# Kernel optimization log

Measured on AMD Instinct MI355X. Metric: run time of the kernel, lower is better.

Reference implementation:

```python
import jax, jax.numpy as jnp
import numpy as np

EPS = 1e-6
TEMPERATURE = 0.1
NEG_INF = -1.0e9

B, S, H = 8, 1024, 1024
M = 16384  # memory_size


def setup_inputs() -> dict:
    key = jax.random.key(0)
    ks = jax.random.split(key, 10)
    sc = 1.0 / np.sqrt(H)
    return {
        "hidden_states": jax.random.normal(ks[0], (B, S, H), jnp.float32),
        "Wk": jax.random.normal(ks[1], (H, H), jnp.float32) * sc,
        "bk": jax.random.normal(ks[2], (H,), jnp.float32) * 0.01,
        "Wv": jax.random.normal(ks[3], (H, H), jnp.float32) * sc,
        "bv": jax.random.normal(ks[4], (H,), jnp.float32) * 0.01,
        "Wo": jax.random.normal(ks[5], (H, H), jnp.float32) * sc,
        "bo": jax.random.normal(ks[6], (H,), jnp.float32) * 0.01,
        "memory_keys": jax.random.normal(ks[7], (M, H), jnp.float32),
        "memory_values": jax.random.normal(ks[8], (M, H), jnp.float32),
        "memory_usage": jax.random.randint(ks[9], (M,), 0, 3, jnp.int32),
    }


def _normalize(x):
    # matches torch: x * rsqrt(sum(x^2) + 1e-6)
    return x * jax.lax.rsqrt(jnp.sum(jnp.square(x), axis=-1, keepdims=True) + EPS)


def reference(hidden_states, Wk, bk, Wv, bv, Wo, bo,
              memory_keys, memory_values, memory_usage):
    # key projection + L2-ish normalization of queries
    q = hidden_states @ Wk.T + bk              # [B,S,H]
    qn = _normalize(q)
    mkn = _normalize(memory_keys)              # [M,H]
    # cosine-similarity attention over memory slots
    scores = jnp.einsum('bsh,mh->bsm', qn, mkn) / TEMPERATURE  # [B,S,M]
    mask = (memory_usage > 0).astype(scores.dtype)             # [M]
    scores = scores * mask + NEG_INF * (1.0 - mask)
    w = jax.nn.softmax(scores, axis=-1)                        # [B,S,M]
    retrieved = jnp.einsum('bsm,mh->bsh', w, memory_values)    # [B,S,H]
    return retrieved @ Wo.T + bo
```

## Files before the change

### kernel.cpp

```cpp
#include <hip/hip_runtime.h>
#include <hip/hip_bf16.h>
#include <stdint.h>
#include <stddef.h>

typedef __bf16 bf16_t;
typedef __attribute__((ext_vector_type(8))) __bf16 bf16x8;
typedef __attribute__((ext_vector_type(4))) __bf16 bf16x4;
typedef __attribute__((ext_vector_type(4))) float f32x4;

#define HDIM 1024
#define MSLOTS 16384
#define NROWS 8192

__device__ __forceinline__ void load16_lds(const void* g, void* l) {
  __builtin_amdgcn_global_load_lds((const __attribute__((address_space(1))) void*)g,
                                   (__attribute__((address_space(3))) void*)l, 16, 0, 0);
}

__global__ void init_compact(int* __restrict__ cmask) {
  int i = blockIdx.x * blockDim.x + threadIdx.x;
  if (i < MSLOTS) cmask[i] = 0;
}

__global__ void compact_scan(const int* __restrict__ usage, int* __restrict__ posmap,
                             int* __restrict__ cmask, int* __restrict__ smalls) {
  __shared__ int wtot[16], wbase[16];
  const int t = threadIdx.x;
  const int lane = t & 63, wid = t >> 6;
  const int base = t * 16;
  unsigned mask = 0;
  int c = 0;
  #pragma unroll
  for (int i = 0; i < 16; ++i) {
    if (usage[base + i] > 0) { mask |= (1u << i); ++c; }
  }
  int inc = c;
  #pragma unroll
  for (int d = 1; d < 64; d <<= 1) {
    int n = __shfl_up(inc, d);
    if (lane >= d) inc += n;
  }
  if (lane == 63) wtot[wid] = inc;
  __syncthreads();
  if (t == 0) {
    int acc = 0;
    #pragma unroll
    for (int w = 0; w < 16; ++w) { wbase[w] = acc; acc += wtot[w]; }
    smalls[0] = acc;
    smalls[1] = ((acc + 511) >> 9) << 9;
  }
  __syncthreads();
  int pos = wbase[wid] + inc - c;
  #pragma unroll
  for (int i = 0; i < 16; ++i) {
    if ((mask >> i) & 1u) {
      posmap[pos] = base + i;
      cmask[pos] = 1;
      ++pos;
    }
  }
}

__global__ void cvt_f32_bf16(const float* __restrict__ X, bf16_t* __restrict__ Y, int n8) {
  int i = blockIdx.x * blockDim.x + threadIdx.x;
  if (i >= n8) return;
  float4 a = ((const float4*)X)[2 * i];
  float4 b = ((const float4*)X)[2 * i + 1];
  bf16x8 o;
  o[0] = (bf16_t)a.x; o[1] = (bf16_t)a.y; o[2] = (bf16_t)a.z; o[3] = (bf16_t)a.w;
  o[4] = (bf16_t)b.x; o[5] = (bf16_t)b.y; o[6] = (bf16_t)b.z; o[7] = (bf16_t)b.w;
  ((bf16x8*)Y)[i] = o;
}

__global__ void normalize_rows(const float* __restrict__ X, bf16_t* __restrict__ Y) {
  __shared__ float part[4];
  const int t = threadIdx.x;
  const size_t row = blockIdx.x;
  float4 v = ((const float4*)(X + row * 1024))[t];
  float s = v.x * v.x + v.y * v.y + v.z * v.z + v.w * v.w;
  #pragma unroll
  for (int m = 32; m >= 1; m >>= 1) s += __shfl_xor(s, m);
  if ((t & 63) == 0) part[t >> 6] = s;
  __syncthreads();
  float tot = part[0] + part[1] + part[2] + part[3];
  float r = rsqrtf(tot + 1e-6f);
  bf16x4 o;
  o[0] = (bf16_t)(v.x * r); o[1] = (bf16_t)(v.y * r);
  o[2] = (bf16_t)(v.z * r); o[3] = (bf16_t)(v.w * r);
  *(bf16x4*)&Y[row * 1024 + t * 4] = o;
}

__global__ void normalize_gather(const float* __restrict__ mk, const int* __restrict__ posmap,
                                 const int* __restrict__ smalls, bf16_t* __restrict__ cmkn) {
  __shared__ float part[4];
  const int p = blockIdx.x;
  const int cnt = smalls[0], mpad = smalls[1];
  if (p >= mpad) return;
  const int t = threadIdx.x;
  if (p >= cnt) {
    bf16x4 z;
    z[0] = z[1] = z[2] = z[3] = (bf16_t)0.f;
    *(bf16x4*)&cmkn[(size_t)p * 1024 + t * 4] = z;
    return;
  }
  const int slot = posmap[p];
  float4 v = ((const float4*)(mk + (size_t)slot * 1024))[t];
  float s = v.x * v.x + v.y * v.y + v.z * v.z + v.w * v.w;
  #pragma unroll
  for (int m = 32; m >= 1; m >>= 1) s += __shfl_xor(s, m);
  if ((t & 63) == 0) part[t >> 6] = s;
  __syncthreads();
  float tot = part[0] + part[1] + part[2] + part[3];
  float r = rsqrtf(tot + 1e-6f);
  bf16x4 o;
  o[0] = (bf16_t)(v.x * r); o[1] = (bf16_t)(v.y * r);
  o[2] = (bf16_t)(v.z * r); o[3] = (bf16_t)(v.w * r);
  *(bf16x4*)&cmkn[(size_t)p * 1024 + t * 4] = o;
}

__global__ void transpose_gather(const float* __restrict__ mv, const int* __restrict__ posmap,
                                 const int* __restrict__ smalls, bf16_t* __restrict__ cVt) {
  __shared__ float tile[32][33];
  const int cnt = smalls[0], mpad = smalls[1];
  const int p0 = blockIdx.y * 32;
  if (p0 >= mpad) return;
  const int tx = threadIdx.x & 31, ty = threadIdx.x >> 5;
  const int h0 = blockIdx.x * 32;
  #pragma unroll
  for (int j = 0; j < 32; j += 8) {
    const int pos = p0 + ty + j;
    float val = 0.f;
    if (pos < cnt) val = mv[(size_t)posmap[pos] * 1024 + h0 + tx];
    tile[ty + j][tx] = val;
  }
  __syncthreads();
  #pragma unroll
  for (int j = 0; j < 32; j += 8)
    cVt[(size_t)(h0 + ty + j) * MSLOTS + p0 + tx] = (bf16_t)tile[tx][ty + j];
}

__global__ void zero_f32(float* __restrict__ p, int n4) {
  int i = blockIdx.x * blockDim.x + threadIdx.x;
  if (i < n4) ((float4*)p)[i] = (float4){0.f, 0.f, 0.f, 0.f};
}

__global__ void scale_cvt(const float* __restrict__ retrf, const float* __restrict__ den,
                          bf16_t* __restrict__ out, int n4) {
  int i = blockIdx.x * blockDim.x + threadIdx.x;
  if (i >= n4) return;
  float4 s = ((const float4*)retrf)[i];
  const int row = (i * 4) >> 10;
  const float r = 1.0f / den[row];
  bf16x4 o;
  o[0] = (bf16_t)(s.x * r); o[1] = (bf16_t)(s.y * r);
  o[2] = (bf16_t)(s.z * r); o[3] = (bf16_t)(s.w * r);
  ((bf16x4*)out)[i] = o;
}

__global__ void reduce_scale(const float* __restrict__ part, size_t partStride, int ks,
                             const float* __restrict__ den, bf16_t* __restrict__ out, int n4) {
  int i = blockIdx.x * blockDim.x + threadIdx.x;
  if (i >= n4) return;
  float4 s = ((const float4*)part)[i];
  for (int k = 1; k < ks; ++k) {
    float4 t = ((const float4*)(part + (size_t)k * partStride))[i];
    s.x += t.x; s.y += t.y; s.z += t.z; s.w += t.w;
  }
  const int row = (i * 4) >> 10;
  const float r = 1.0f / den[row];
  bf16x4 o;
  o[0] = (bf16_t)(s.x * r); o[1] = (bf16_t)(s.y * r);
  o[2] = (bf16_t)(s.z * r); o[3] = (bf16_t)(s.w * r);
  ((bf16x4*)out)[i] = o;
}

template <int EPI>
__global__ void gemm_bt(const bf16_t* __restrict__ A, const bf16_t* __restrict__ Bt,
                        int ldk, int kLenIn, int ldc,
                        const float* __restrict__ bias,
                        const int* __restrict__ cmask,
                        float* __restrict__ den,
                        float* __restrict__ outf, bf16_t* __restrict__ outb,
                        const int* __restrict__ smalls, int ks, size_t partStride) {
  __shared__ bf16_t lA[128 * 32];
  __shared__ bf16_t lB[128 * 32];
  const int t = threadIdx.x;
  const int lane = t & 63;
  const int wave = t >> 6;
  const int wm = (wave >> 1) << 6;
  const int wn = (wave & 1) << 6;
  const int lr = lane & 15;
  const int lq = lane >> 4;

  int bx = blockIdx.x, by = blockIdx.y, bz = blockIdx.z;
  {
    const unsigned nx = gridDim.x, ny = gridDim.y;
    if ((ny & 7u) == 0u) {
      unsigned lin = blockIdx.x + nx * (blockIdx.y + ny * blockIdx.z);
      unsigned ylow = lin & 7u;
      lin >>= 3;
      const unsigned nyh = ny >> 3;
      unsigned yhigh = lin % nyh;
      lin /= nyh;
      bx = lin % nx;
      bz = lin / nx;
      by = ylow + 8u * yhigh;
    }
  }

  int kLen = kLenIn;
  int kstart = 0;
  if (EPI == 1) {
    if (bx * 128 >= smalls[1]) return;
  }
  if (EPI == 3 || EPI == 4) {
    kLen = smalls[1] / ks;
    kstart = bz * kLen;
  }

  const int r0 = t >> 2;
  const int c0 = (t & 3) * 8;
  const bf16_t* pA0 = A + (size_t)(by * 128 + r0) * ldk + kstart + c0;
  const bf16_t* pA1 = pA0 + (size_t)64 * ldk;
  const bf16_t* pB0 = Bt + (size_t)(bx * 128 + r0) * ldk + kstart + c0;
  const bf16_t* pB1 = pB0 + (size_t)64 * ldk;

  f32x4 acc[4][4];
  #pragma unroll
  for (int i = 0; i < 4; ++i)
    #pragma unroll
    for (int j = 0; j < 4; ++j) acc[i][j] = (f32x4){0.f, 0.f, 0.f, 0.f};

  for (int k0 = 0; k0 < kLen; k0 += 32) {
    __syncthreads();
    load16_lds(pA0, &lA[t * 8]);
    load16_lds(pA1, &lA[2048 + t * 8]);
    load16_lds(pB0, &lB[t * 8]);
    load16_lds(pB1, &lB[2048 + t * 8]);
    pA0 += 32; pA1 += 32; pB0 += 32; pB1 += 32;
    __syncthreads();
    bf16x8 af[4], bfr[4];
    #pragma unroll
    for (int i = 0; i < 4; ++i)
      af[i] = *(const bf16x8*)&lA[(wm + i * 16 + lr) * 32 + lq * 8];
    #pragma unroll
    for (int j = 0; j < 4; ++j)
      bfr[j] = *(const bf16x8*)&lB[(wn + j * 16 + lr) * 32 + lq * 8];
    #pragma unroll
    for (int i = 0; i < 4; ++i)
      #pragma unroll
      for (int j = 0; j < 4; ++j)
        acc[i][j] = __builtin_amdgcn_mfma_f32_16x16x32_bf16(af[i], bfr[j], acc[i][j], 0, 0, 0);
  }

  const int colBase = bx * 128 + wn + lr;
  const int rowBase = by * 128 + wm + lq * 4;

  if (EPI == 4) outf += (size_t)bz * partStride;

  float rs[4][4];
  if (EPI == 1) {
    #pragma unroll
    for (int i = 0; i < 4; ++i)
      #pragma unroll
      for (int r = 0; r < 4; ++r) rs[i][r] = 0.f;
  }

  #pragma unroll
  for (int j = 0; j < 4; ++j) {
    const int col = colBase + j * 16;
    float bval = 0.f;
    bool ok = true;
    if (EPI == 0) bval = bias[col];
    if (EPI == 1) ok = cmask[col] > 0;
    #pragma unroll
    for (int i = 0; i < 4; ++i) {
      const int row = rowBase + i * 16;
      #pragma unroll
      for (int r = 0; r < 4; ++r) {
        const size_t idx = (size_t)(row + r) * ldc + col;
        float v = acc[i][j][r];
        if (EPI == 0) outf[idx] = v + bval;
        if (EPI == 1) {
          float e = ok ? exp2f(v * 14.426950408889634f) : 0.f;
          rs[i][r] += e;
          outb[idx] = (bf16_t)e;
        }
        if (EPI == 3) atomicAdd(&outf[idx], v);
        if (EPI == 4) outf[idx] = v;
      }
    }
  }

  if (EPI == 1) {
    #pragma unroll
    for (int i = 0; i < 4; ++i)
      #pragma unroll
      for (int r = 0; r < 4; ++r) {
        float s = rs[i][r];
        s += __shfl_xor(s, 1);
        s += __shfl_xor(s, 2);
        s += __shfl_xor(s, 4);
        s += __shfl_xor(s, 8);
        if (lr == 0) atomicAdd(&den[rowBase + i * 16 + r], s);
      }
  }
}

extern "C" void kernel_launch(void* const* d_in, const int* in_sizes, int n_in,
                              void* d_out, int out_size, void* d_ws, size_t ws_size,
                              hipStream_t stream) {
  const float* hs = (const float*)d_in[0];
  const float* Wk = (const float*)d_in[1];
  const float* bk = (const float*)d_in[2];
  const float* Wo = (const float*)d_in[5];
  const float* bo = (const float*)d_in[6];
  const float* mk = (const float*)d_in[7];
  const float* mv = (const float*)d_in[8];
  const int* usage = (const int*)d_in[9];
  float* out = (float*)d_out;

  char* ws = (char*)d_ws;
  size_t off = 0;
  auto alloc = [&](size_t b) -> void* {
    void* p = ws + off;
    off += (b + 255) & ~(size_t)255;
    return p;
  };
  bf16_t* cmkn = (bf16_t*)alloc((size_t)MSLOTS * HDIM * 2);
  bf16_t* cVt = (bf16_t*)alloc((size_t)HDIM * MSLOTS * 2);
  bf16_t* qnb = (bf16_t*)alloc((size_t)NROWS * HDIM * 2);
  bf16_t* retrb = (bf16_t*)alloc((size_t)NROWS * HDIM * 2);
  bf16_t* Wob = (bf16_t*)alloc((size_t)HDIM * HDIM * 2);
  float* den = (float*)alloc((size_t)NROWS * 4);
  int* posmap = (int*)alloc((size_t)MSLOTS * 4);
  int* cmask = (int*)alloc((size_t)MSLOTS * 4);
  int* smalls = (int*)alloc(256 * 4);
  const size_t fixed = off;

  int chunk = 128, ksplit = 4, partialMode = 0;
  {
    const int cc[8] = {4096, 4096, 2048, 2048, 1024, 1024, 512, 128};
    const int kk[8] = {4, 4, 8, 8, 8, 8, 16, 4};
    const int pp[8] = {1, 0, 1, 0, 1, 0, 0, 0};
    for (int ci = 0; ci < 8; ++ci) {
      size_t outBytes = pp[ci] ? (size_t)cc[ci] * HDIM * 4 * kk[ci] : (size_t)cc[ci] * HDIM * 4;
      size_t region = (size_t)cc[ci] * MSLOTS * 2 + outBytes;
      size_t phaseA = (size_t)NROWS * HDIM * 2 + (size_t)HDIM * HDIM * 2 +
                      (size_t)NROWS * HDIM * 4 + 1024;
      if (region < phaseA) region = phaseA;
      if (fixed + region <= ws_size) {
        chunk = cc[ci]; ksplit = kk[ci]; partialMode = pp[ci];
        break;
      }
    }
  }
  bf16_t* hsb = (bf16_t*)(ws + fixed);
  bf16_t* Wkb = (bf16_t*)(ws + fixed + (size_t)NROWS * HDIM * 2);
  float* qf = (float*)(ws + fixed + (size_t)NROWS * HDIM * 2 + (size_t)HDIM * HDIM * 2);
  bf16_t* P = (bf16_t*)(ws + fixed);
  float* retrf = (float*)(ws + fixed + (size_t)chunk * MSLOTS * 2);
  const size_t partStride = (size_t)chunk * HDIM;

  init_compact<<<MSLOTS / 256, 256, 0, stream>>>(cmask);
  compact_scan<<<1, 1024, 0, stream>>>(usage, posmap, cmask, smalls);
  cvt_f32_bf16<<<(NROWS * HDIM / 8 + 255) / 256, 256, 0, stream>>>(hs, hsb, NROWS * HDIM / 8);
  cvt_f32_bf16<<<(HDIM * HDIM / 8 + 255) / 256, 256, 0, stream>>>(Wk, Wkb, HDIM * HDIM / 8);
  cvt_f32_bf16<<<(HDIM * HDIM / 8 + 255) / 256, 256, 0, stream>>>(Wo, Wob, HDIM * HDIM / 8);
  normalize_gather<<<MSLOTS, 256, 0, stream>>>(mk, posmap, smalls, cmkn);
  transpose_gather<<<dim3(HDIM / 32, MSLOTS / 32), 256, 0, stream>>>(mv, posmap, smalls, cVt);

  gemm_bt<0><<<dim3(HDIM / 128, NROWS / 128), 256, 0, stream>>>(
      hsb, Wkb, HDIM, HDIM, HDIM, bk, nullptr, nullptr, qf, nullptr, smalls, 1, 0);
  normalize_rows<<<NROWS, 256, 0, stream>>>(qf, qnb);

  for (int c = 0; c < NROWS; c += chunk) {
    zero_f32<<<(chunk / 4 + 255) / 256, 256, 0, stream>>>(den, chunk / 4);
    gemm_bt<1><<<dim3(MSLOTS / 128, chunk / 128), 256, 0, stream>>>(
        qnb + (size_t)c * HDIM, cmkn, HDIM, HDIM, MSLOTS, nullptr, cmask, den, nullptr, P,
        smalls, 1, 0);
    if (partialMode) {
      gemm_bt<4><<<dim3(HDIM / 128, chunk / 128, ksplit), 256, 0, stream>>>(
          P, cVt, MSLOTS, 0, HDIM, nullptr, nullptr, nullptr, retrf, nullptr, smalls, ksplit,
          partStride);
      reduce_scale<<<(chunk * HDIM / 4 + 255) / 256, 256, 0, stream>>>(
          retrf, partStride, ksplit, den, retrb + (size_t)c * HDIM, chunk * HDIM / 4);
    } else {
      zero_f32<<<(chunk * HDIM / 4 + 255) / 256, 256, 0, stream>>>(retrf, chunk * HDIM / 4);
      gemm_bt<3><<<dim3(HDIM / 128, chunk / 128, ksplit), 256, 0, stream>>>(
          P, cVt, MSLOTS, 0, HDIM, nullptr, nullptr, nullptr, retrf, nullptr, smalls, ksplit,
          0);
      scale_cvt<<<(chunk * HDIM / 4 + 255) / 256, 256, 0, stream>>>(
          retrf, den, retrb + (size_t)c * HDIM, chunk * HDIM / 4);
    }
  }

  gemm_bt<0><<<dim3(HDIM / 128, NROWS / 128), 256, 0, stream>>>(
      retrb, Wob, HDIM, HDIM, HDIM, bo, nullptr, nullptr, out, nullptr, smalls, 1, 0);
}
```

Before: 837.7 us.

## Store split-K partials as bf16, aggregate softmax denominators in LDS, trim launches

The split-K partial outputs of the P·V GEMM are written as bf16 instead of fp32, and a new reduce kernel sums eight bf16 values per thread. This halves partial-buffer traffic and lets larger chunks fit in the workspace. Row-sum denominators are first combined in shared memory, so each block issues one global atomic per row. The cmask zeroing moves into compact_scan, and the Wo conversion reuses scratch space at the end. Rounding partials to bf16 before summation adds precision loss.

```diff
diff --git a/kernel.cpp b/kernel.cpp
--- a/kernel.cpp
+++ b/kernel.cpp
@@ -15,11 +15,6 @@
 __device__ __forceinline__ void load16_lds(const void* g, void* l) {
   __builtin_amdgcn_global_load_lds((const __attribute__((address_space(1))) void*)g,
                                    (__attribute__((address_space(3))) void*)l, 16, 0, 0);
-}
-
-__global__ void init_compact(int* __restrict__ cmask) {
-  int i = blockIdx.x * blockDim.x + threadIdx.x;
-  if (i < MSLOTS) cmask[i] = 0;
 }
 
 __global__ void compact_scan(const int* __restrict__ usage, int* __restrict__ posmap,
@@ -27,6 +22,8 @@
   __shared__ int wtot[16], wbase[16];
   const int t = threadIdx.x;
   const int lane = t & 63, wid = t >> 6;
+  for (int i = t; i < MSLOTS; i += 1024) cmask[i] = 0;
+  __syncthreads();
   const int base = t * 16;
   unsigned mask = 0;
   int c = 0;
@@ -157,21 +154,25 @@
   ((bf16x4*)out)[i] = o;
 }
 
-__global__ void reduce_scale(const float* __restrict__ part, size_t partStride, int ks,
-                             const float* __restrict__ den, bf16_t* __restrict__ out, int n4) {
+__global__ void reduce_scale_b(const bf16_t* __restrict__ part, size_t partStride, int ks,
+                               const float* __restrict__ den, bf16_t* __restrict__ out,
+                               int n8) {
   int i = blockIdx.x * blockDim.x + threadIdx.x;
-  if (i >= n4) return;
-  float4 s = ((const float4*)part)[i];
-  for (int k = 1; k < ks; ++k) {
-    float4 t = ((const float4*)(part + (size_t)k * partStride))[i];
-    s.x += t.x; s.y += t.y; s.z += t.z; s.w += t.w;
-  }
-  const int row = (i * 4) >> 10;
+  if (i >= n8) return;
+  float acc[8];
+  #pragma unroll
+  for (int e = 0; e < 8; ++e) acc[e] = 0.f;
+  for (int k = 0; k < ks; ++k) {
+    bf16x8 v = ((const bf16x8*)(part + (size_t)k * partStride))[i];
+    #pragma unroll
+    for (int e = 0; e < 8; ++e) acc[e] += (float)v[e];
+  }
+  const int row = (i * 8) >> 10;
   const float r = 1.0f / den[row];
-  bf16x4 o;
-  o[0] = (bf16_t)(s.x * r); o[1] = (bf16_t)(s.y * r);
-  o[2] = (bf16_t)(s.z * r); o[3] = (bf16_t)(s.w * r);
-  ((bf16x4*)out)[i] = o;
+  bf16x8 o;
+  #pragma unroll
+  for (int e = 0; e < 8; ++e) o[e] = (bf16_t)(acc[e] * r);
+  ((bf16x8*)out)[i] = o;
 }
 
 template <int EPI>
@@ -184,6 +185,7 @@
                         const int* __restrict__ smalls, int ks, size_t partStride) {
   __shared__ bf16_t lA[128 * 32];
   __shared__ bf16_t lB[128 * 32];
+  __shared__ float sden[128];
   const int t = threadIdx.x;
   const int lane = t & 63;
   const int wave = t >> 6;
@@ -256,7 +258,7 @@
   const int colBase = bx * 128 + wn + lr;
   const int rowBase = by * 128 + wm + lq * 4;
 
-  if (EPI == 4) outf += (size_t)bz * partStride;
+  if (EPI == 4) outb += (size_t)bz * partStride;
 
   float rs[4][4];
   if (EPI == 1) {
@@ -287,12 +289,14 @@
           outb[idx] = (bf16_t)e;
         }
         if (EPI == 3) atomicAdd(&outf[idx], v);
-        if (EPI == 4) outf[idx] = v;
+        if (EPI == 4) outb[idx] = (bf16_t)v;
       }
     }
   }
 
   if (EPI == 1) {
+    if (t < 128) sden[t] = 0.f;
+    __syncthreads();
     #pragma unroll
     for (int i = 0; i < 4; ++i)
       #pragma unroll
@@ -302,8 +306,10 @@
         s += __shfl_xor(s, 2);
         s += __shfl_xor(s, 4);
         s += __shfl_xor(s, 8);
-        if (lr == 0) atomicAdd(&den[rowBase + i * 16 + r], s);
+        if (lr == 0) atomicAdd(&sden[wm + i * 16 + lq * 4 + r], s);
       }
+    __syncthreads();
+    if (t < 128) atomicAdd(&den[by * 128 + t], sden[t]);
   }
 }
 
@@ -331,26 +337,26 @@
   bf16_t* cVt = (bf16_t*)alloc((size_t)HDIM * MSLOTS * 2);
   bf16_t* qnb = (bf16_t*)alloc((size_t)NROWS * HDIM * 2);
   bf16_t* retrb = (bf16_t*)alloc((size_t)NROWS * HDIM * 2);
-  bf16_t* Wob = (bf16_t*)alloc((size_t)HDIM * HDIM * 2);
   float* den = (float*)alloc((size_t)NROWS * 4);
   int* posmap = (int*)alloc((size_t)MSLOTS * 4);
   int* cmask = (int*)alloc((size_t)MSLOTS * 4);
   int* smalls = (int*)alloc(256 * 4);
   const size_t fixed = off;
 
-  int chunk = 128, ksplit = 4, partialMode = 0;
+  int chunk = 128, ksplit = 4, modePB = 0;
   {
-    const int cc[8] = {4096, 4096, 2048, 2048, 1024, 1024, 512, 128};
-    const int kk[8] = {4, 4, 8, 8, 8, 8, 16, 4};
-    const int pp[8] = {1, 0, 1, 0, 1, 0, 0, 0};
+    const int cc[8] = {4096, 2048, 4096, 2048, 1024, 1024, 512, 128};
+    const int kk[8] = {4, 8, 4, 8, 8, 8, 16, 4};
+    const int pb[8] = {1, 1, 0, 0, 1, 0, 0, 0};
+    const size_t phaseA = (size_t)NROWS * HDIM * 2 + (size_t)HDIM * HDIM * 2 +
+                          (size_t)NROWS * HDIM * 4 + 1024;
     for (int ci = 0; ci < 8; ++ci) {
-      size_t outBytes = pp[ci] ? (size_t)cc[ci] * HDIM * 4 * kk[ci] : (size_t)cc[ci] * HDIM * 4;
+      size_t outBytes = pb[ci] ? (size_t)cc[ci] * HDIM * 2 * kk[ci]
+                               : (size_t)cc[ci] * HDIM * 4;
       size_t region = (size_t)cc[ci] * MSLOTS * 2 + outBytes;
-      size_t phaseA = (size_t)NROWS * HDIM * 2 + (size_t)HDIM * HDIM * 2 +
-                      (size_t)NROWS * HDIM * 4 + 1024;
       if (region < phaseA) region = phaseA;
       if (fixed + region <= ws_size) {
-        chunk = cc[ci]; ksplit = kk[ci]; partialMode = pp[ci];
+        chunk = cc[ci]; ksplit = kk[ci]; modePB = pb[ci];
         break;
       }
     }
@@ -359,14 +365,15 @@
   bf16_t* Wkb = (bf16_t*)(ws + fixed + (size_t)NROWS * HDIM * 2);
   float* qf = (float*)(ws + fixed + (size_t)NROWS * HDIM * 2 + (size_t)HDIM * HDIM * 2);
   bf16_t* P = (bf16_t*)(ws + fixed);
-  float* retrf = (float*)(ws + fixed + (size_t)chunk * MSLOTS * 2);
+  char* after = ws + fixed + (size_t)chunk * MSLOTS * 2;
+  bf16_t* retrh = (bf16_t*)after;
+  float* retrf = (float*)after;
+  bf16_t* Wob = (bf16_t*)(ws + fixed);
   const size_t partStride = (size_t)chunk * HDIM;
 
-  init_compact<<<MSLOTS / 256, 256, 0, stream>>>(cmask);
   compact_scan<<<1, 1024, 0, stream>>>(usage, posmap, cmask, smalls);
   cvt_f32_bf16<<<(NROWS * HDIM / 8 + 255) / 256, 256, 0, stream>>>(hs, hsb, NROWS * HDIM / 8);
   cvt_f32_bf16<<<(HDIM * HDIM / 8 + 255) / 256, 256, 0, stream>>>(Wk, Wkb, HDIM * HDIM / 8);
-  cvt_f32_bf16<<<(HDIM * HDIM / 8 + 255) / 256, 256, 0, stream>>>(Wo, Wob, HDIM * HDIM / 8);
   normalize_gather<<<MSLOTS, 256, 0, stream>>>(mk, posmap, smalls, cmkn);
   transpose_gather<<<dim3(HDIM / 32, MSLOTS / 32), 256, 0, stream>>>(mv, posmap, smalls, cVt);
 
@@ -379,12 +386,12 @@
     gemm_bt<1><<<dim3(MSLOTS / 128, chunk / 128), 256, 0, stream>>>(
         qnb + (size_t)c * HDIM, cmkn, HDIM, HDIM, MSLOTS, nullptr, cmask, den, nullptr, P,
         smalls, 1, 0);
-    if (partialMode) {
+    if (modePB) {
       gemm_bt<4><<<dim3(HDIM / 128, chunk / 128, ksplit), 256, 0, stream>>>(
-          P, cVt, MSLOTS, 0, HDIM, nullptr, nullptr, nullptr, retrf, nullptr, smalls, ksplit,
+          P, cVt, MSLOTS, 0, HDIM, nullptr, nullptr, nullptr, nullptr, retrh, smalls, ksplit,
           partStride);
-      reduce_scale<<<(chunk * HDIM / 4 + 255) / 256, 256, 0, stream>>>(
-          retrf, partStride, ksplit, den, retrb + (size_t)c * HDIM, chunk * HDIM / 4);
+      reduce_scale_b<<<(chunk * HDIM / 8 + 255) / 256, 256, 0, stream>>>(
+          retrh, partStride, ksplit, den, retrb + (size_t)c * HDIM, chunk * HDIM / 8);
     } else {
       zero_f32<<<(chunk * HDIM / 4 + 255) / 256, 256, 0, stream>>>(retrf, chunk * HDIM / 4);
       gemm_bt<3><<<dim3(HDIM / 128, chunk / 128, ksplit), 256, 0, stream>>>(
@@ -395,6 +402,7 @@
     }
   }
 
+  cvt_f32_bf16<<<(HDIM * HDIM / 8 + 255) / 256, 256, 0, stream>>>(Wo, Wob, HDIM * HDIM / 8);
   gemm_bt<0><<<dim3(HDIM / 128, NROWS / 128), 256, 0, stream>>>(
       retrb, Wob, HDIM, HDIM, HDIM, bo, nullptr, nullptr, out, nullptr, smalls, 1, 0);
 }
```

After: 846.0 us. No clear change (+1.0%).
